# Optimization experiments

Measured on AMD Instinct MI355X. Metric: run time of the kernel, lower is better.

The kernel has to match this reference:

```python
import jax, jax.numpy as jnp
from jax import lax
import numpy as np

K_IN, K_OUT, H, ML = 32, 16, 256, 80
L_PRE, L_FWD, B = 60, 80, 1024


def gru_cell(x, h, Wih, Whh, bih, bhh):
    # torch GRU gate order: r, z, n
    gi = x @ Wih.T + bih
    gh = h @ Whh.T + bhh
    ir, iz, inn = jnp.split(gi, 3, axis=-1)
    hr, hz, hn = jnp.split(gh, 3, axis=-1)
    r = jax.nn.sigmoid(ir + hr)
    z = jax.nn.sigmoid(iz + hz)
    n = jnp.tanh(inn + r * hn)
    return (1.0 - z) * n + z * h


def setup_inputs() -> dict:
    key = jax.random.key(0)
    ks = jax.random.split(key, 24)
    s = 0.05
    rn = lambda k, shp: (jax.random.normal(k, shp) * s).astype(jnp.float32)
    inp = {
        "pre_x": jax.random.normal(ks[0], (L_PRE, B, K_IN), dtype=jnp.float32),
        "pre_y": jax.random.normal(ks[1], (L_PRE, B, K_OUT), dtype=jnp.float32),
        "forward_x": jax.random.normal(ks[2], (L_FWD, B, K_IN), dtype=jnp.float32),
        # encoder: embedding Linear(k_in+k_out -> H), GRU(H,H)
        "enc_emb_W": rn(ks[3], (H, K_IN + K_OUT)),
        "enc_emb_b": rn(ks[4], (H,)),
        "enc_Wih": rn(ks[5], (3 * H, H)),
        "enc_Whh": rn(ks[6], (3 * H, H)),
        "enc_bih": rn(ks[7], (3 * H,)),
        "enc_bhh": rn(ks[8], (3 * H,)),
        # decoder: embedding Linear(k_out+k_in -> H), attn Linear(2H -> ML),
        # attn_combine Linear(2H -> H), GRU(H,H), out Linear(H -> k_out)
        "dec_emb_W": rn(ks[9], (H, K_OUT + K_IN)),
        "dec_emb_b": rn(ks[10], (H,)),
        "attn_W": rn(ks[11], (ML, 2 * H)),
        "attn_b": rn(ks[12], (ML,)),
        "comb_W": rn(ks[13], (H, 2 * H)),
        "comb_b": rn(ks[14], (H,)),
        "dec_Wih": rn(ks[15], (3 * H, H)),
        "dec_Whh": rn(ks[16], (3 * H, H)),
        "dec_bih": rn(ks[17], (3 * H,)),
        "dec_bhh": rn(ks[18], (3 * H,)),
        "out_W": rn(ks[19], (K_OUT, H)),
        "out_b": rn(ks[20], (K_OUT,)),
    }
    return inp


def reference(pre_x, pre_y, forward_x,
              enc_emb_W, enc_emb_b, enc_Wih, enc_Whh, enc_bih, enc_bhh,
              dec_emb_W, dec_emb_b, attn_W, attn_b, comb_W, comb_b,
              dec_Wih, dec_Whh, dec_bih, dec_bhh, out_W, out_b):
    L_pre, batch, _ = pre_x.shape
    hdim = enc_emb_b.shape[0]
    max_len = attn_b.shape[0]

    # ---- encoder ----
    emb = jnp.concatenate([pre_x, pre_y], axis=2) @ enc_emb_W.T + enc_emb_b  # [L_pre,B,H]
    h0 = jnp.zeros((batch, hdim), dtype=pre_x.dtype)

    def enc_step(h, x):
        h2 = gru_cell(x, h, enc_Wih, enc_Whh, enc_bih, enc_bhh)
        return h2, h2

    enc_h, enc_outs = lax.scan(enc_step, h0, emb)
    # pad encoder outputs to max_length along time (zeros beyond L_pre)
    enc_outputs = jnp.zeros((max_len, batch, hdim), dtype=pre_x.dtype).at[:L_pre].set(enc_outs)
    enc_bmh = enc_outputs.transpose(1, 0, 2)  # [B, ML, H]

    # ---- decoder (dropout inactive: eval mode) ----
    def dec_step(carry, fx):
        y, h = carry
        di = jnp.concatenate([y, fx], axis=-1)            # [B, k_out+k_in]
        e = di @ dec_emb_W.T + dec_emb_b                   # [B, H]
        logits = jnp.concatenate([e, h], axis=-1) @ attn_W.T + attn_b  # [B, ML]
        aw = jax.nn.softmax(logits, axis=-1)
        ctx = jnp.einsum('bm,bmh->bh', aw, enc_bmh)        # [B, H]
        g = jnp.tanh(jnp.concatenate([e, ctx], axis=-1) @ comb_W.T + comb_b)
        h2 = gru_cell(g, h, dec_Wih, dec_Whh, dec_bih, dec_bhh)
        y2 = h2 @ out_W.T + out_b                          # [B, k_out]
        return (y2, h2), y2

    y_init = jnp.zeros_like(pre_y[0])
    _, ys = lax.scan(dec_step, (y_init, enc_h), forward_x)
    return ys  # [L_fwd, B, k_out]
```

## Files before the change

kernel.cpp:

```cpp
#include <hip/hip_runtime.h>
#include <hip/hip_bf16.h>

#define BATCH 1024
#define HD 256
#define MLEN 80
#define LPRE 60
#define LFWD 80
#define KIN 32
#define KOUT 16

typedef unsigned short bf16_t;
typedef __attribute__((ext_vector_type(8))) short bf16x8;
typedef __attribute__((ext_vector_type(4))) float f32x4;
typedef __attribute__((ext_vector_type(4))) unsigned u32x4;

#define MFMA __builtin_amdgcn_mfma_f32_16x16x32_bf16

__device__ __forceinline__ float bf2f(bf16_t v){ return __uint_as_float(((unsigned)v)<<16); }
__device__ __forceinline__ bf16_t f2bf(float f){
    unsigned u = __float_as_uint(f);
    return (bf16_t)((u + 0x7FFFu + ((u>>16)&1u)) >> 16);
}
__device__ __forceinline__ unsigned pack2(float lo, float hi){
    return (unsigned)f2bf(lo) | ((unsigned)f2bf(hi)<<16);
}
__device__ __forceinline__ float bflo(unsigned d){ return __uint_as_float(d<<16); }
__device__ __forceinline__ float bfhi(unsigned d){ return __uint_as_float(d & 0xffff0000u); }
__device__ __forceinline__ float sigm(float x){ return 1.0f/(1.0f+__expf(-x)); }

#define OFF_Z  262144
#define OFF_IN 524288
#define OFF_HN 655360

__global__ void pack_gru(const float* __restrict__ Wih, const float* __restrict__ Whh,
                         bf16_t* __restrict__ dst)
{
    int T = blockIdx.x*256 + threadIdx.x;
    int grp, local;
    if (T < 16384){ grp=0; local=T; }
    else if (T < 32768){ grp=1; local=T-16384; }
    else if (T < 40960){ grp=2; local=T-32768; }
    else { grp=3; local=T-40960; }
    int nkt = (grp<2)?16:8;
    int nt  = local / (nkt*64);
    int rem = local - nt*(nkt*64);
    int kt  = rem >> 6;
    int l   = rem & 63;
    int n   = nt*16 + (l&15);
    int k0  = kt*32 + ((l>>4)<<3);
    unsigned w[4];
    #pragma unroll
    for (int h2=0; h2<4; h2++){
        float v[2];
        #pragma unroll
        for (int s=0; s<2; s++){
            int k = k0 + h2*2 + s;
            if (grp==0)      v[s] = (k<256)? Wih[(size_t)n*HD + k]       : Whh[(size_t)n*HD + (k-256)];
            else if (grp==1) v[s] = (k<256)? Wih[(size_t)(256+n)*HD + k] : Whh[(size_t)(256+n)*HD + (k-256)];
            else if (grp==2) v[s] = Wih[(size_t)(512+n)*HD + k];
            else             v[s] = Whh[(size_t)(512+n)*HD + k];
        }
        w[h2] = pack2(v[0], v[1]);
    }
    uint4 u = {w[0],w[1],w[2],w[3]};
    *(uint4*)((char*)dst + (size_t)T*16) = u;
}

__global__ void pack_B512(const float* __restrict__ W, bf16_t* __restrict__ dst)
{
    int T = blockIdx.x*256 + threadIdx.x;
    int nt = T >> 10, kt = (T>>6)&15, l = T&63;
    int n = nt*16 + (l&15);
    int k0 = kt*32 + ((l>>4)<<3);
    unsigned w[4];
    #pragma unroll
    for (int h2=0; h2<4; h2++)
        w[h2] = pack2(W[(size_t)n*512 + k0+h2*2], W[(size_t)n*512 + k0+h2*2+1]);
    uint4 u = {w[0],w[1],w[2],w[3]};
    *(uint4*)((char*)dst + (size_t)T*16) = u;
}

__global__ void wfuse_kernel(const float* __restrict__ dembW, const float* __restrict__ dembB,
                             const float* __restrict__ outW, const float* __restrict__ outB,
                             float* __restrict__ Wfuse, float* __restrict__ ebias)
{
    int T = blockIdx.x*256 + threadIdx.x;
    if (T < 65536){
        int k = T >> 8, n = T & 255;
        float acc = 0.f;
        #pragma unroll
        for (int o=0;o<16;o++) acc += dembW[(size_t)n*48 + o]*outW[(size_t)o*HD + k];
        Wfuse[(size_t)k*HD + n] = acc;
    } else if (T < 65792){
        int n = T - 65536;
        float acc = dembB[n];
        #pragma unroll
        for (int o=0;o<16;o++) acc += outB[o]*dembW[(size_t)n*48 + o];
        ebias[n] = acc;
    }
}

__global__ void pack_e(const float* __restrict__ Wfuse, const float* __restrict__ dembW,
                       bf16_t* __restrict__ dst)
{
    int T = blockIdx.x*256 + threadIdx.x;
    int nt = T/576, rem = T - nt*576;
    int kt = rem >> 6, l = rem & 63;
    int n = nt*16 + (l&15);
    int k0 = kt*32 + ((l>>4)<<3);
    unsigned w[4];
    #pragma unroll
    for (int h2=0; h2<4; h2++){
        float v[2];
        #pragma unroll
        for (int s=0;s<2;s++){
            int k = k0 + h2*2 + s;
            v[s] = (kt<8)? Wfuse[(size_t)k*HD + n] : dembW[(size_t)n*48 + 16 + (k-256)];
        }
        w[h2] = pack2(v[0], v[1]);
    }
    uint4 u = {w[0],w[1],w[2],w[3]};
    *(uint4*)((char*)dst + (size_t)T*16) = u;
}

__global__ void pack_logits(const float* __restrict__ Wfuse, const float* __restrict__ dembW,
                            const float* __restrict__ attW, const float* __restrict__ attB,
                            const float* __restrict__ dembB, const float* __restrict__ ebias,
                            bf16_t* __restrict__ BL, bf16_t* __restrict__ BL0,
                            float* __restrict__ lb, float* __restrict__ lb0)
{
    int T = blockIdx.x*256 + threadIdx.x;
    if (T < 5760){
        int variant = (T < 2880) ? 0 : 1;
        int local = variant ? (T-2880) : T;
        int nt = local/576, rem = local - nt*576;
        int kt = rem >> 6, l = rem & 63;
        int m  = nt*16 + (l&15);
        int k0 = kt*32 + ((l>>4)<<3);
        unsigned w[4];
        #pragma unroll
        for (int h2=0; h2<4; h2++){
            float v[2];
            for (int s=0;s<2;s++){
                int k = k0 + h2*2 + s;
                float acc;
                if (kt < 8){
                    if (variant == 0){
                        acc = attW[(size_t)m*512 + 256 + k];
                        for (int n=0;n<256;n++) acc += Wfuse[(size_t)k*HD + n]*attW[(size_t)m*512 + n];
                    } else {
                        acc = attW[(size_t)m*512 + 256 + k];
                    }
                } else {
                    int kp = k - 256;
                    acc = 0.f;
                    for (int n=0;n<256;n++) acc += dembW[(size_t)n*48 + 16 + kp]*attW[(size_t)m*512 + n];
                }
                v[s] = acc;
            }
            w[h2] = pack2(v[0], v[1]);
        }
        uint4 u = {w[0],w[1],w[2],w[3]};
        bf16_t* d = variant ? BL0 : BL;
        *(uint4*)((char*)d + (size_t)local*16) = u;
    } else if (T < 5840){
        int m = T - 5760;
        float acc = attB[m];
        for (int n=0;n<256;n++) acc += ebias[n]*attW[(size_t)m*512 + n];
        lb[m] = acc;
    } else if (T < 5920){
        int m = T - 5840;
        float acc = attB[m];
        for (int n=0;n<256;n++) acc += dembB[n]*attW[(size_t)m*512 + n];
        lb0[m] = acc;
    }
}

__global__ void pack_out(const float* __restrict__ outW, bf16_t* __restrict__ dst)
{
    int T = blockIdx.x*256 + threadIdx.x;
    int kt = T >> 6, l = T & 63;
    int n  = l & 15;
    int k0 = kt*32 + ((l>>4)<<3);
    unsigned w[4];
    #pragma unroll
    for (int h2=0; h2<4; h2++)
        w[h2] = pack2(outW[(size_t)n*HD + k0+h2*2], outW[(size_t)n*HD + k0+h2*2+1]);
    uint4 u = {w[0],w[1],w[2],w[3]};
    *(uint4*)((char*)dst + (size_t)T*16) = u;
}

__global__ __launch_bounds__(256) void emb_kernel(
    const float* __restrict__ px, const float* __restrict__ py,
    const float* __restrict__ embW, const float* __restrict__ embB,
    bf16_t* __restrict__ emb)
{
    __shared__ float Ws[256*49];
    __shared__ float xy[16][48];
    __shared__ float bs[256];
    int t = blockIdx.y, b0 = blockIdx.x*16, tid = threadIdx.x;
    for (int i = tid; i < 256*48; i += 256){ int n=i/48, k=i-n*48; Ws[n*49+k]=embW[i]; }
    bs[tid] = embB[tid];
    for (int i = tid; i < 16*48; i += 256){
        int r=i/48, k=i-r*48;
        xy[r][k] = (k<KIN)? px[((size_t)t*BATCH + b0+r)*KIN + k]
                          : py[((size_t)t*BATCH + b0+r)*KOUT + (k-KIN)];
    }
    __syncthreads();
    int n = tid;
    const float* w = &Ws[n*49];
    for (int r=0;r<16;r++){
        float acc = bs[n];
        #pragma unroll
        for (int k=0;k<48;k++) acc += xy[r][k]*w[k];
        emb[((size_t)t*BATCH + b0+r)*HD + n] = f2bf(acc);
    }
}

__global__ void fxconv(const float* __restrict__ fx, bf16_t* __restrict__ dst)
{
    size_t i = (size_t)blockIdx.x*256 + threadIdx.x;
    const float4* s = (const float4*)(fx + i*8);
    float4 a = s[0], b = s[1];
    uint4 u = { pack2(a.x,a.y), pack2(a.z,a.w), pack2(b.x,b.y), pack2(b.z,b.w) };
    *(uint4*)(dst + i*8) = u;
}

__global__ __launch_bounds__(256) void gru_step(
    const bf16_t* __restrict__ A0, const bf16_t* __restrict__ A1,
    const bf16_t* __restrict__ Bp,
    const float* __restrict__ bih, const float* __restrict__ bhh,
    const float* __restrict__ hprev, float* __restrict__ hnext,
    bf16_t* __restrict__ hnext_bf, bf16_t* __restrict__ extra_bf)
{
    __shared__ __align__(16) bf16_t As[16][520];
    int tid = threadIdx.x, b0 = blockIdx.x*16;
    for (int i = tid; i < 1024; i += 256){
        int r = i>>6, c = i&63;
        const bf16_t* src = (c<32)? (A0 + (size_t)(b0+r)*HD + c*8)
                                  : (A1 + (size_t)(b0+r)*HD + (c-32)*8);
        *(uint4*)&As[r][c*8] = *(const uint4*)src;
    }
    __syncthreads();
    int lane = tid & 63, wave = tid >> 6;
    int jt = blockIdx.y*4 + wave;
    const char* arow = (const char*)&As[lane&15][(lane>>4)*8];
    const char* bpc = (const char*)Bp;
    size_t loff = (size_t)lane*16;
    f32x4 cr={0,0,0,0}, cz={0,0,0,0}, ci={0,0,0,0}, ch={0,0,0,0};
    #pragma unroll
    for (int kt=0; kt<16; kt++){
        bf16x8 a  = *(const bf16x8*)(arow + kt*64);
        bf16x8 br = *(const bf16x8*)(bpc + (size_t)(((jt<<4)+kt)<<10) + loff);
        bf16x8 bz = *(const bf16x8*)(bpc + OFF_Z + (size_t)(((jt<<4)+kt)<<10) + loff);
        cr = MFMA(a, br, cr, 0,0,0);
        cz = MFMA(a, bz, cz, 0,0,0);
        if (kt < 8){
            bf16x8 bi = *(const bf16x8*)(bpc + OFF_IN + (size_t)(((jt<<3)+kt)<<10) + loff);
            ci = MFMA(a, bi, ci, 0,0,0);
        } else {
            bf16x8 bh = *(const bf16x8*)(bpc + OFF_HN + (size_t)(((jt<<3)+kt-8)<<10) + loff);
            ch = MFMA(a, bh, ch, 0,0,0);
        }
    }
    int j = (jt<<4) + (lane&15);
    float b_r = bih[j] + bhh[j];
    float b_z = bih[256+j] + bhh[256+j];
    float b_i = bih[512+j], b_h = bhh[512+j];
    #pragma unroll
    for (int q=0;q<4;q++){
        int b = b0 + ((lane>>4)<<2) + q;
        float rv = sigm(cr[q] + b_r);
        float zv = sigm(cz[q] + b_z);
        float nv = tanhf(ci[q] + b_i + rv*(ch[q] + b_h));
        float h2 = (1.0f - zv)*nv + zv*hprev[(size_t)b*HD + j];
        hnext[(size_t)b*HD + j] = h2;
        bf16_t hb = f2bf(h2);
        hnext_bf[(size_t)b*HD + j] = hb;
        extra_bf[(size_t)b*HD + j] = hb;
    }
}

__global__ __launch_bounds__(1024) void dec_front(
    const bf16_t* __restrict__ hbf, const bf16_t* __restrict__ fxt,
    const bf16_t* __restrict__ enc_out,
    const bf16_t* __restrict__ Be, const bf16_t* __restrict__ BL,
    const bf16_t* __restrict__ Bcmb, const bf16_t* __restrict__ Bout,
    const float* __restrict__ ebp, const float* __restrict__ lbp,
    const float* __restrict__ combB, const float* __restrict__ outB,
    int t, bf16_t* __restrict__ g_out, float* __restrict__ out)
{
    __shared__ __align__(16) bf16_t As[16][296];
    __shared__ __align__(16) bf16_t Eb[16][264];
    __shared__ __align__(16) bf16_t Cb[16][264];
    __shared__ float awL[16][84];
    __shared__ float Cpart[16][256];

    int tid = threadIdx.x, b0 = blockIdx.x*16;

    if (tid < 576){
        int r = tid/36, c = tid - r*36;
        const bf16_t* src = (c<32)? (hbf + (size_t)(b0+r)*HD + c*8)
                                  : (fxt + (size_t)(b0+r)*KIN + (c-32)*8);
        *(uint4*)&As[r][c*8] = *(const uint4*)src;
    }

    int half = tid >> 9;
    int u    = tid & 511;
    int cr_  = u >> 5;
    int cc0  = (u & 31) * 8;
    const bf16_t* cbp = enc_out + ((size_t)(half*30)*BATCH + (b0+cr_))*HD + cc0;
    u32x4 pf[10];
    #pragma unroll
    for (int i=0;i<10;i++) pf[i] = *(const u32x4*)(cbp + (size_t)i*BATCH*HD);

    __syncthreads();

    int lane = tid & 63, wave = tid >> 6;
    const bf16_t* arow = &As[lane&15][(lane>>4)*8];
    size_t loff = (size_t)lane*16;
    int ke0 = t ? 0 : 8;

    {
        f32x4 c = {0,0,0,0};
        for (int kt = ke0; kt < 9; kt++){
            bf16x8 a = *(const bf16x8*)(arow + kt*32);
            bf16x8 b = *(const bf16x8*)((const char*)Be + (size_t)((wave*9+kt)<<10) + loff);
            c = MFMA(a, b, c, 0,0,0);
        }
        int n = (wave<<4) + (lane&15);
        float bbn = ebp[n];
        #pragma unroll
        for (int q=0;q<4;q++) Eb[((lane>>4)<<2)+q][n] = f2bf(c[q] + bbn);
    }
    if (wave < 5){
        f32x4 c = {0,0,0,0};
        #pragma unroll
        for (int kt = 0; kt < 9; kt++){
            bf16x8 a = *(const bf16x8*)(arow + kt*32);
            bf16x8 b = *(const bf16x8*)((const char*)BL + (size_t)((wave*9+kt)<<10) + loff);
            c = MFMA(a, b, c, 0,0,0);
        }
        int m = (wave<<4) + (lane&15);
        float bbm = lbp[m];
        #pragma unroll
        for (int q=0;q<4;q++) awL[((lane>>4)<<2)+q][m] = c[q] + bbm;
    } else if (wave == 5 && t > 0){
        f32x4 c = {0,0,0,0};
        #pragma unroll
        for (int kt = 0; kt < 8; kt++){
            bf16x8 a = *(const bf16x8*)(arow + kt*32);
            bf16x8 b = *(const bf16x8*)((const char*)Bout + (size_t)(kt<<10) + loff);
            c = MFMA(a, b, c, 0,0,0);
        }
        int o = lane & 15;
        float bo = outB[o];
        #pragma unroll
        for (int q=0;q<4;q++){
            int r = ((lane>>4)<<2) + q;
            out[((size_t)(t-1)*BATCH + b0+r)*KOUT + o] = c[q] + bo;
        }
    }
    __syncthreads();

    if (tid < 256){
        int r2 = tid >> 4, l2 = tid & 15;
        float vmax = -1e30f;
        for (int m=l2; m<80; m+=16) vmax = fmaxf(vmax, awL[r2][m]);
        #pragma unroll
        for (int k=1; k<16; k<<=1) vmax = fmaxf(vmax, __shfl_xor(vmax, k, 16));
        float ps = 0.f;
        for (int m=l2; m<80; m+=16){ float v = __expf(awL[r2][m]-vmax); awL[r2][m]=v; ps += v; }
        #pragma unroll
        for (int k=1; k<16; k<<=1) ps += __shfl_xor(ps, k, 16);
        float inv = 1.0f/ps;
        for (int m=l2; m<80; m+=16) awL[r2][m] *= inv;
    }
    __syncthreads();

    float acc[8];
    #pragma unroll
    for (int i=0;i<8;i++) acc[i] = 0.f;
    {
        const float* awr = &awL[cr_][half*30];
        #pragma unroll
        for (int i=0;i<10;i++){
            float w = awr[i];
            acc[0] = fmaf(w, bflo(pf[i][0]), acc[0]);
            acc[1] = fmaf(w, bfhi(pf[i][0]), acc[1]);
            acc[2] = fmaf(w, bflo(pf[i][1]), acc[2]);
            acc[3] = fmaf(w, bfhi(pf[i][1]), acc[3]);
            acc[4] = fmaf(w, bflo(pf[i][2]), acc[4]);
            acc[5] = fmaf(w, bfhi(pf[i][2]), acc[5]);
            acc[6] = fmaf(w, bflo(pf[i][3]), acc[6]);
            acc[7] = fmaf(w, bfhi(pf[i][3]), acc[7]);
        }
        #pragma unroll 5
        for (int i=10;i<30;i++){
            u32x4 v = *(const u32x4*)(cbp + (size_t)i*BATCH*HD);
            float w = awr[i];
            acc[0] = fmaf(w, bflo(v[0]), acc[0]);
            acc[1] = fmaf(w, bfhi(v[0]), acc[1]);
            acc[2] = fmaf(w, bflo(v[1]), acc[2]);
            acc[3] = fmaf(w, bfhi(v[1]), acc[3]);
            acc[4] = fmaf(w, bflo(v[2]), acc[4]);
            acc[5] = fmaf(w, bfhi(v[2]), acc[5]);
            acc[6] = fmaf(w, bflo(v[3]), acc[6]);
            acc[7] = fmaf(w, bfhi(v[3]), acc[7]);
        }
    }
    if (half == 0){
        float4 p0 = {acc[0],acc[1],acc[2],acc[3]};
        float4 p1 = {acc[4],acc[5],acc[6],acc[7]};
        *(float4*)&Cpart[cr_][cc0]   = p0;
        *(float4*)&Cpart[cr_][cc0+4] = p1;
    }
    __syncthreads();

    if (half == 1){
        float4 p0 = *(const float4*)&Cpart[cr_][cc0];
        float4 p1 = *(const float4*)&Cpart[cr_][cc0+4];
        uint4 ov;
        ov.x = pack2(acc[0]+p0.x, acc[1]+p0.y);
        ov.y = pack2(acc[2]+p0.z, acc[3]+p0.w);
        ov.z = pack2(acc[4]+p1.x, acc[5]+p1.y);
        ov.w = pack2(acc[6]+p1.z, acc[7]+p1.w);
        *(uint4*)&Cb[cr_][cc0] = ov;
    }
    __syncthreads();

    {
        const bf16_t* ae = &Eb[lane&15][(lane>>4)*8];
        const bf16_t* ac = &Cb[lane&15][(lane>>4)*8];
        f32x4 c = {0,0,0,0};
        #pragma unroll
        for (int kt=0; kt<16; kt++){
            bf16x8 a = (kt<8)? *(const bf16x8*)(ae + kt*32)
                             : *(const bf16x8*)(ac + (kt-8)*32);
            bf16x8 b = *(const bf16x8*)((const char*)Bcmb + (size_t)(((wave<<4)+kt)<<10) + loff);
            c = MFMA(a, b, c, 0,0,0);
        }
        int n = (wave<<4) + (lane&15);
        float bbn = combB[n];
        #pragma unroll
        for (int q=0;q<4;q++){
            int r = ((lane>>4)<<2) + q;
            g_out[(size_t)(b0+r)*HD + n] = f2bf(tanhf(c[q] + bbn));
        }
    }
}

__global__ __launch_bounds__(256) void final79(
    const float* __restrict__ hf, const float* __restrict__ outW,
    const float* __restrict__ outB, float* __restrict__ ys)
{
    __shared__ float hs[16][260];
    __shared__ float ow[16*260];
    int tid = threadIdx.x, b0 = blockIdx.x*16;
    for (int i=tid;i<4096;i+=256){ int o2=i>>8,k=i&255; ow[o2*260+k]=outW[(size_t)o2*HD+k]; }
    for (int i=tid;i<4096;i+=256){ int r=i>>8,k=i&255; hs[r][k]=hf[(size_t)(b0+r)*HD+k]; }
    __syncthreads();
    int r=tid>>4, o=tid&15;
    float acc=outB[o];
    const float* w=&ow[o*260];
    for(int k=0;k<256;k++) acc += hs[r][k]*w[k];
    ys[((size_t)79*BATCH + b0+r)*KOUT + o] = acc;
}

extern "C" void kernel_launch(void* const* d_in, const int* in_sizes, int n_in,
                              void* d_out, int out_size, void* d_ws, size_t ws_size,
                              hipStream_t stream) {
    const float* pre_x    = (const float*)d_in[0];
    const float* pre_y    = (const float*)d_in[1];
    const float* fwd_x    = (const float*)d_in[2];
    const float* enc_embW = (const float*)d_in[3];
    const float* enc_embB = (const float*)d_in[4];
    const float* enc_Wih  = (const float*)d_in[5];
    const float* enc_Whh  = (const float*)d_in[6];
    const float* enc_bih  = (const float*)d_in[7];
    const float* enc_bhh  = (const float*)d_in[8];
    const float* dec_embW = (const float*)d_in[9];
    const float* dec_embB = (const float*)d_in[10];
    const float* attn_W   = (const float*)d_in[11];
    const float* attn_b   = (const float*)d_in[12];
    const float* comb_W   = (const float*)d_in[13];
    const float* comb_b   = (const float*)d_in[14];
    const float* dec_Wih  = (const float*)d_in[15];
    const float* dec_Whh  = (const float*)d_in[16];
    const float* dec_bih  = (const float*)d_in[17];
    const float* dec_bhh  = (const float*)d_in[18];
    const float* out_W    = (const float*)d_in[19];
    const float* out_b    = (const float*)d_in[20];
    float* out = (float*)d_out;

    char* ws = (char*)d_ws;
    size_t o = 0;
    auto alloc = [&](size_t bytes)->char*{
        char* p = ws + o; o = (o + bytes + 255) & ~(size_t)255; return p;
    };
    bf16_t* EMB     = (bf16_t*)alloc((size_t)LPRE*BATCH*HD*2);
    bf16_t* ENC_OUT = (bf16_t*)alloc((size_t)LPRE*BATCH*HD*2);
    bf16_t* FXB     = (bf16_t*)alloc((size_t)LFWD*BATCH*KIN*2);
    float*  HF0     = (float*) alloc((size_t)BATCH*HD*4);
    float*  HF1     = (float*) alloc((size_t)BATCH*HD*4);
    bf16_t* HB0     = (bf16_t*)alloc((size_t)BATCH*HD*2);
    bf16_t* HB1     = (bf16_t*)alloc((size_t)BATCH*HD*2);
    bf16_t* GBUF    = (bf16_t*)alloc((size_t)BATCH*HD*2);
    bf16_t* DUMMY   = (bf16_t*)alloc((size_t)BATCH*HD*2);
    float*  WFUSE   = (float*) alloc((size_t)256*256*4);
    float*  EBIAS   = (float*) alloc(256*4);
    float*  LB      = (float*) alloc(80*4);
    float*  LB0     = (float*) alloc(80*4);
    bf16_t* PACK_ENC = (bf16_t*)alloc(786432);
    bf16_t* PACK_DEC = (bf16_t*)alloc(786432);
    bf16_t* PACK_CMB = (bf16_t*)alloc(262144);
    bf16_t* PACK_E   = (bf16_t*)alloc(147456);
    bf16_t* PACK_BL  = (bf16_t*)alloc(46080);
    bf16_t* PACK_BL0 = (bf16_t*)alloc(46080);
    bf16_t* PACK_OUT = (bf16_t*)alloc(8192);

    hipMemsetAsync(HF0, 0, (size_t)BATCH*HD*4, stream);
    hipMemsetAsync(HB0, 0, (size_t)BATCH*HD*2, stream);

    dim3 blk(256);
    emb_kernel<<<dim3(64,60), blk, 0, stream>>>(pre_x, pre_y, enc_embW, enc_embB, EMB);
    fxconv<<<dim3(1280), blk, 0, stream>>>(fwd_x, FXB);
    pack_gru<<<dim3(192), blk, 0, stream>>>(enc_Wih, enc_Whh, PACK_ENC);
    pack_gru<<<dim3(192), blk, 0, stream>>>(dec_Wih, dec_Whh, PACK_DEC);
    pack_B512<<<dim3(64), blk, 0, stream>>>(comb_W, PACK_CMB);
    wfuse_kernel<<<dim3(257), blk, 0, stream>>>(dec_embW, dec_embB, out_W, out_b, WFUSE, EBIAS);
    pack_e<<<dim3(36), blk, 0, stream>>>(WFUSE, dec_embW, PACK_E);
    pack_logits<<<dim3(24), blk, 0, stream>>>(WFUSE, dec_embW, attn_W, attn_b, dec_embB,
                                              EBIAS, PACK_BL, PACK_BL0, LB, LB0);
    pack_out<<<dim3(2), blk, 0, stream>>>(out_W, PACK_OUT);

    float*  HF[2] = {HF0, HF1};
    bf16_t* HB[2] = {HB0, HB1};
    int p = 0;

    for (int t = 0; t < LPRE; t++){
        gru_step<<<dim3(64,4), blk, 0, stream>>>(
            EMB + (size_t)t*BATCH*HD, HB[p], PACK_ENC, enc_bih, enc_bhh,
            HF[p], HF[p^1], HB[p^1], ENC_OUT + (size_t)t*BATCH*HD);
        p ^= 1;
    }
    for (int t = 0; t < LFWD; t++){
        const bf16_t* fxt = FXB + (size_t)t*BATCH*KIN;
        dec_front<<<dim3(64), dim3(1024), 0, stream>>>(
            HB[p], fxt, ENC_OUT,
            PACK_E, t ? PACK_BL : PACK_BL0, PACK_CMB, PACK_OUT,
            t ? EBIAS : dec_embB, t ? LB : LB0, comb_b, out_b,
            t, GBUF, out);
        gru_step<<<dim3(64,4), blk, 0, stream>>>(
            GBUF, HB[p], PACK_DEC, dec_bih, dec_bhh,
            HF[p], HF[p^1], HB[p^1], DUMMY);
        p ^= 1;
    }
    final79<<<dim3(64), blk, 0, stream>>>(HF[p], out_W, out_b, out);
}
```

Baseline: 2.480 ms.

## Split GRU step K-reduction across wave pairs with LDS reduction

```diff
diff --git a/kernel.cpp b/kernel.cpp
--- a/kernel.cpp
+++ b/kernel.cpp
@@ -226,7 +226,7 @@
     *(uint4*)(dst + i*8) = u;
 }
 
-__global__ __launch_bounds__(256) void gru_step(
+__global__ __launch_bounds__(512) void gru_step2(
     const bf16_t* __restrict__ A0, const bf16_t* __restrict__ A1,
     const bf16_t* __restrict__ Bp,
     const float* __restrict__ bih, const float* __restrict__ bhh,
@@ -234,8 +234,11 @@
     bf16_t* __restrict__ hnext_bf, bf16_t* __restrict__ extra_bf)
 {
     __shared__ __align__(16) bf16_t As[16][520];
+    __shared__ __align__(16) f32x4 redR[4][64];
+    __shared__ __align__(16) f32x4 redZ[4][64];
+    __shared__ __align__(16) f32x4 redI[4][64];
     int tid = threadIdx.x, b0 = blockIdx.x*16;
-    for (int i = tid; i < 1024; i += 256){
+    for (int i = tid; i < 1024; i += 512){
         int r = i>>6, c = i&63;
         const bf16_t* src = (c<32)? (A0 + (size_t)(b0+r)*HD + c*8)
                                   : (A1 + (size_t)(b0+r)*HD + (c-32)*8);
@@ -243,41 +246,51 @@
     }
     __syncthreads();
     int lane = tid & 63, wave = tid >> 6;
-    int jt = blockIdx.y*4 + wave;
+    int pairId = wave >> 1, half = wave & 1;
+    int jt = blockIdx.y*4 + pairId;
     const char* arow = (const char*)&As[lane&15][(lane>>4)*8];
     const char* bpc = (const char*)Bp;
     size_t loff = (size_t)lane*16;
-    f32x4 cr={0,0,0,0}, cz={0,0,0,0}, ci={0,0,0,0}, ch={0,0,0,0};
-    #pragma unroll
-    for (int kt=0; kt<16; kt++){
+    size_t offX = half ? (size_t)OFF_HN : (size_t)OFF_IN;
+    int kt0 = half*8;
+    f32x4 cr={0,0,0,0}, cz={0,0,0,0}, cx={0,0,0,0};
+    #pragma unroll
+    for (int k8=0; k8<8; k8++){
+        int kt = kt0 + k8;
         bf16x8 a  = *(const bf16x8*)(arow + kt*64);
         bf16x8 br = *(const bf16x8*)(bpc + (size_t)(((jt<<4)+kt)<<10) + loff);
         bf16x8 bz = *(const bf16x8*)(bpc + OFF_Z + (size_t)(((jt<<4)+kt)<<10) + loff);
+        bf16x8 bx = *(const bf16x8*)(bpc + offX + (size_t)(((jt<<3)+k8)<<10) + loff);
         cr = MFMA(a, br, cr, 0,0,0);
         cz = MFMA(a, bz, cz, 0,0,0);
-        if (kt < 8){
-            bf16x8 bi = *(const bf16x8*)(bpc + OFF_IN + (size_t)(((jt<<3)+kt)<<10) + loff);
-            ci = MFMA(a, bi, ci, 0,0,0);
-        } else {
-            bf16x8 bh = *(const bf16x8*)(bpc + OFF_HN + (size_t)(((jt<<3)+kt-8)<<10) + loff);
-            ch = MFMA(a, bh, ch, 0,0,0);
-        }
-    }
-    int j = (jt<<4) + (lane&15);
-    float b_r = bih[j] + bhh[j];
-    float b_z = bih[256+j] + bhh[256+j];
-    float b_i = bih[512+j], b_h = bhh[512+j];
-    #pragma unroll
-    for (int q=0;q<4;q++){
-        int b = b0 + ((lane>>4)<<2) + q;
-        float rv = sigm(cr[q] + b_r);
-        float zv = sigm(cz[q] + b_z);
-        float nv = tanhf(ci[q] + b_i + rv*(ch[q] + b_h));
-        float h2 = (1.0f - zv)*nv + zv*hprev[(size_t)b*HD + j];
-        hnext[(size_t)b*HD + j] = h2;
-        bf16_t hb = f2bf(h2);
-        hnext_bf[(size_t)b*HD + j] = hb;
-        extra_bf[(size_t)b*HD + j] = hb;
+        cx = MFMA(a, bx, cx, 0,0,0);
+    }
+    if (half == 0){
+        redR[pairId][lane] = cr;
+        redZ[pairId][lane] = cz;
+        redI[pairId][lane] = cx;
+    }
+    __syncthreads();
+    if (half == 1){
+        f32x4 crA = redR[pairId][lane];
+        f32x4 czA = redZ[pairId][lane];
+        f32x4 ci  = redI[pairId][lane];
+        int j = (jt<<4) + (lane&15);
+        float b_r = bih[j] + bhh[j];
+        float b_z = bih[256+j] + bhh[256+j];
+        float b_i = bih[512+j], b_h = bhh[512+j];
+        #pragma unroll
+        for (int q=0;q<4;q++){
+            int b = b0 + ((lane>>4)<<2) + q;
+            float rv = sigm(cr[q] + crA[q] + b_r);
+            float zv = sigm(cz[q] + czA[q] + b_z);
+            float nv = tanhf(ci[q] + b_i + rv*(cx[q] + b_h));
+            float h2 = (1.0f - zv)*nv + zv*hprev[(size_t)b*HD + j];
+            hnext[(size_t)b*HD + j] = h2;
+            bf16_t hb = f2bf(h2);
+            hnext_bf[(size_t)b*HD + j] = hb;
+            extra_bf[(size_t)b*HD + j] = hb;
+        }
     }
 }
 
@@ -539,7 +552,7 @@
     int p = 0;
 
     for (int t = 0; t < LPRE; t++){
-        gru_step<<<dim3(64,4), blk, 0, stream>>>(
+        gru_step2<<<dim3(64,4), dim3(512), 0, stream>>>(
             EMB + (size_t)t*BATCH*HD, HB[p], PACK_ENC, enc_bih, enc_bhh,
             HF[p], HF[p^1], HB[p^1], ENC_OUT + (size_t)t*BATCH*HD);
         p ^= 1;
@@ -551,7 +564,7 @@
             PACK_E, t ? PACK_BL : PACK_BL0, PACK_CMB, PACK_OUT,
             t ? EBIAS : dec_embB, t ? LB : LB0, comb_b, out_b,
             t, GBUF, out);
-        gru_step<<<dim3(64,4), blk, 0, stream>>>(
+        gru_step2<<<dim3(64,4), dim3(512), 0, stream>>>(
             GBUF, HB[p], PACK_DEC, dec_bih, dec_bhh,
             HF[p], HF[p^1], HB[p^1], DUMMY);
         p ^= 1;
```

New measurement: 2.462 ms. No clear change (-0.7%).
